# Kernel optimization log

Hardware: AMD Instinct MI355X
Metric: run time of the kernel (lower is better)

Reference implementation:

```python
import jax, jax.numpy as jnp
import numpy as np

B, N, ND, H = 8, 1024, 64, 128
NUM_OPS, NUM_PARAMS, SKETCH = 64, 256, 128


def setup_inputs() -> dict:
    key = jax.random.key(0)
    ks = iter(jax.random.split(key, 64))

    def rn(shape, s=0.05):
        return jax.random.normal(next(ks), shape, dtype=jnp.float32) * s

    inp = {
        'node_features': jax.random.normal(next(ks), (B, N, ND), dtype=jnp.float32),
        'adjacency': (jax.random.uniform(next(ks), (B, N, N)) < 0.05).astype(jnp.float32),
        'mask': jnp.ones((B, N), jnp.float32),
    }
    for name, din in (('g1', ND), ('g2', H), ('g3', H)):
        inp[name + '_W'] = rn((din, H))
        inp[name + '_b'] = jnp.zeros((H,), jnp.float32)
        inp[name + '_aW'] = rn((2 * H,))
        inp[name + '_ab'] = jnp.zeros((), jnp.float32)
    for l in (0, 1):
        inp[f'l{l}_Wih'] = rn((4 * H, H))
        inp[f'l{l}_Whh'] = rn((4 * H, H))
        inp[f'l{l}_bih'] = jnp.zeros((4 * H,), jnp.float32)
        inp[f'l{l}_bhh'] = jnp.zeros((4 * H,), jnp.float32)
    for name, dout in (('op', NUM_OPS), ('pa', NUM_PARAMS), ('sk', SKETCH), ('no', ND)):
        inp[name + '_W1'] = rn((H, H))
        inp[name + '_b1'] = jnp.zeros((H,), jnp.float32)
        inp[name + '_W2'] = rn((H, dout))
        inp[name + '_b2'] = jnp.zeros((dout,), jnp.float32)
    return inp


def _gnn(x, adj, W, b, aW, ab):
    # h = Linear(x); att[b,i,j] = sigmoid(aW . [h_j ; h_i] + ab)  (cat order from the torch code)
    h = x @ W + b                      # [B,N,H]
    D = W.shape[1]
    sj = h @ aW[:D]                    # contribution of the dim-1-expanded term (h_j)
    si = h @ aW[D:]                    # contribution of the dim-2-expanded term (h_i)
    att = jax.nn.sigmoid(si[:, :, None] + sj[:, None, :] + ab) * adj  # [B,N,N]
    return jnp.einsum('bij,bjd->bid', att, h)


def _lstm(x, Wih, Whh, bih, bhh):
    # single torch-style LSTM layer, gate order i,f,g,o; zero initial state
    Bx, Hh = x.shape[0], Whh.shape[1]

    def step(carry, xt):
        h, c = carry
        g = xt @ Wih.T + h @ Whh.T + (bih + bhh)       # [B,4H]
        i, f, gg, o = jnp.split(g, 4, axis=-1)
        c = jax.nn.sigmoid(f) * c + jax.nn.sigmoid(i) * jnp.tanh(gg)
        h = jax.nn.sigmoid(o) * jnp.tanh(c)
        return (h, c), h

    z = jnp.zeros((Bx, Hh), x.dtype)
    _, ys = jax.lax.scan(step, (z, z), jnp.swapaxes(x, 0, 1))
    return jnp.swapaxes(ys, 0, 1)


def _mlp(x, W1, b1, W2, b2):
    return jax.nn.relu(x @ W1 + b1) @ W2 + b2


def reference(node_features, adjacency, mask,
              g1_W, g1_b, g1_aW, g1_ab,
              g2_W, g2_b, g2_aW, g2_ab,
              g3_W, g3_b, g3_aW, g3_ab,
              l0_Wih, l0_Whh, l0_bih, l0_bhh,
              l1_Wih, l1_Whh, l1_bih, l1_bhh,
              op_W1, op_b1, op_W2, op_b2,
              pa_W1, pa_b1, pa_W2, pa_b2,
              sk_W1, sk_b1, sk_W2, sk_b2,
              no_W1, no_b1, no_W2, no_b2):
    h = jax.nn.relu(_gnn(node_features, adjacency, g1_W, g1_b, g1_aW, g1_ab))
    h = jax.nn.relu(_gnn(h, adjacency, g2_W, g2_b, g2_aW, g2_ab))
    h = _gnn(h, adjacency, g3_W, g3_b, g3_aW, g3_ab)
    lo = _lstm(h, l0_Wih, l0_Whh, l0_bih, l0_bhh)
    lo = _lstm(lo, l1_Wih, l1_Whh, l1_bih, l1_bhh)
    op_pred = _mlp(lo, op_W1, op_b1, op_W2, op_b2)
    param_pred = _mlp(lo, pa_W1, pa_b1, pa_W2, pa_b2)
    sketch_pred = _mlp(lo, sk_W1, sk_b1, sk_W2, sk_b2)
    node_pred = _mlp(h, no_W1, no_b1, no_W2, no_b2)
    return (op_pred, param_pred, sketch_pred, node_pred)
```

## Files before the change

### kernel.cpp

```cpp
#include <hip/hip_runtime.h>

typedef __attribute__((ext_vector_type(8))) short short8;
typedef __attribute__((ext_vector_type(4))) float f32x4;
typedef __attribute__((ext_vector_type(2))) float f32x2;
typedef __attribute__((ext_vector_type(4))) unsigned short us4;
typedef __attribute__((ext_vector_type(2))) unsigned int u32x2;

__device__ __forceinline__ unsigned short bf16_of(float f) {
    unsigned u = __builtin_bit_cast(unsigned, f);
    u += 0x7fffu + ((u >> 16) & 1u);
    return (unsigned short)(u >> 16);
}
__device__ __forceinline__ unsigned bf16pk(float a, float b) {
    return (unsigned)bf16_of(a) | ((unsigned)bf16_of(b) << 16);
}
__device__ __forceinline__ float fexp2(float x) { return __builtin_amdgcn_exp2f(x); }
__device__ __forceinline__ float frcp(float x) { return __builtin_amdgcn_rcpf(x); }
__device__ __forceinline__ float sigm(float x) { return frcp(1.f + fexp2(-1.44269504f * x)); }
__device__ __forceinline__ float tanh_f(float x) {
    float e = fexp2(2.88539008f * x);
    return 1.f - 2.f * frcp(e + 1.f);
}
__device__ __forceinline__ f32x4 mfma16(short8 a, short8 b, f32x4 c) {
    return __builtin_amdgcn_mfma_f32_16x16x32_bf16(a, b, c, 0, 0, 0);
}
__device__ __forceinline__ float dpp_shr8(float x) {
    return __builtin_bit_cast(float, __builtin_amdgcn_update_dpp(
        0, __builtin_bit_cast(int, x), 0x118, 0xF, 0xF, true));
}
__device__ __forceinline__ float dpp_shl8(float x) {
    return __builtin_bit_cast(float, __builtin_amdgcn_update_dpp(
        0, __builtin_bit_cast(int, x), 0x108, 0xF, 0xF, true));
}

__global__ __launch_bounds__(256) void gemm_f32(
    const float* __restrict__ A, const float* __restrict__ B,
    const float* __restrict__ bias, float* __restrict__ C,
    int M, int N, int K, int BT, int RELU, int PACK)
{
    __shared__ float As[64][33];
    __shared__ float Bs[32][68];
    const int tid = threadIdx.x;
    const int tx = tid & 15, ty = tid >> 4;
    const int m0 = blockIdx.y * 64, n0 = blockIdx.x * 64;
    float acc[4][4];
#pragma unroll
    for (int i = 0; i < 4; ++i)
#pragma unroll
        for (int j = 0; j < 4; ++j) acc[i][j] = 0.f;

    for (int k0 = 0; k0 < K; k0 += 32) {
        __syncthreads();
        {
            const int r = tid >> 2, kk = (tid & 3) * 8;
            const float* src = A + (size_t)(m0 + r) * K + k0 + kk;
            f32x4 v0 = *(const f32x4*)src;
            f32x4 v1 = *(const f32x4*)(src + 4);
#pragma unroll
            for (int e = 0; e < 4; ++e) { As[r][kk + e] = v0[e]; As[r][kk + 4 + e] = v1[e]; }
        }
        if (!BT) {
            const int kk = tid >> 3, nn = (tid & 7) * 8;
            const float* src = B + (size_t)(k0 + kk) * N + n0 + nn;
            f32x4 v0 = *(const f32x4*)src;
            f32x4 v1 = *(const f32x4*)(src + 4);
#pragma unroll
            for (int e = 0; e < 4; ++e) { Bs[kk][nn + e] = v0[e]; Bs[kk][nn + 4 + e] = v1[e]; }
        } else {
            const int n = tid >> 2, kk = (tid & 3) * 8;
            const float* src = B + (size_t)(n0 + n) * K + k0 + kk;
            f32x4 v0 = *(const f32x4*)src;
            f32x4 v1 = *(const f32x4*)(src + 4);
#pragma unroll
            for (int e = 0; e < 4; ++e) { Bs[kk + e][n] = v0[e]; Bs[kk + 4 + e][n] = v1[e]; }
        }
        __syncthreads();
#pragma unroll 8
        for (int k = 0; k < 32; ++k) {
            float a0 = As[ty * 4 + 0][k], a1 = As[ty * 4 + 1][k];
            float a2 = As[ty * 4 + 2][k], a3 = As[ty * 4 + 3][k];
            f32x4 bv = *(const f32x4*)&Bs[k][tx * 4];
#pragma unroll
            for (int j = 0; j < 4; ++j) {
                acc[0][j] += a0 * bv[j]; acc[1][j] += a1 * bv[j];
                acc[2][j] += a2 * bv[j]; acc[3][j] += a3 * bv[j];
            }
        }
    }
    f32x4 bv = {};
    if (bias != nullptr) bv = *(const f32x4*)&bias[n0 + tx * 4];
#pragma unroll
    for (int i = 0; i < 4; ++i) {
        f32x4 res = {};
#pragma unroll
        for (int j = 0; j < 4; ++j) {
            float v = acc[i][j] + bv[j];
            if (RELU) v = fmaxf(v, 0.f);
            res[j] = v;
        }
        const int m = m0 + ty * 4 + i;
        if (!PACK) {
            *(f32x4*)&C[(size_t)m * N + n0 + tx * 4] = res;
        } else {
            const int b = m >> 10, t = m & 1023;
            const int n = n0 + tx * 4;
            const int pr = n >> 7, h = n & 127;
            *(f32x4*)&C[(((size_t)t * 4 + pr) * 8 + b) * 128 + h] = res;
        }
    }
}

__global__ __launch_bounds__(256) void sisj_kernel(
    const float* __restrict__ h, const float* __restrict__ aW,
    float* __restrict__ si, float* __restrict__ sj)
{
    const int tid = threadIdx.x, lane = tid & 63, w = tid >> 6;
    const int row = blockIdx.x * 4 + w;
    f32x2 hv = *(const f32x2*)(h + (size_t)row * 128 + lane * 2);
    f32x2 w1 = *(const f32x2*)&aW[lane * 2];
    f32x2 w2 = *(const f32x2*)&aW[128 + lane * 2];
    float sjp = hv[0] * w1[0] + hv[1] * w1[1];
    float sip = hv[0] * w2[0] + hv[1] * w2[1];
#pragma unroll
    for (int o = 32; o > 0; o >>= 1) {
        sjp += __shfl_xor(sjp, o);
        sip += __shfl_xor(sip, o);
    }
    if (lane == 0) { si[row] = sip; sj[row] = sjp; }
}

__global__ __launch_bounds__(256) void transpose_bf16_k(
    const float* __restrict__ h, unsigned short* __restrict__ hT)
{
    __shared__ float t[64][65];
    const int b = blockIdx.z, jt = blockIdx.x, dt = blockIdx.y;
    const int tid = threadIdx.x;
    const int r = tid >> 4, c4 = (tid & 15) * 4;
#pragma unroll
    for (int rr = 0; rr < 4; ++rr) {
        const int j = rr * 16 + r;
        f32x4 v = *(const f32x4*)(h + ((size_t)b * 1024 + jt * 64 + j) * 128 + dt * 64 + c4);
#pragma unroll
        for (int e = 0; e < 4; ++e) t[j][c4 + e] = v[e];
    }
    __syncthreads();
#pragma unroll
    for (int rr = 0; rr < 4; ++rr) {
        const int d = rr * 16 + r;
        u32x2 o;
        o[0] = bf16pk(t[c4 + 0][d], t[c4 + 1][d]);
        o[1] = bf16pk(t[c4 + 2][d], t[c4 + 3][d]);
        *(u32x2*)(hT + ((size_t)b * 128 + dt * 64 + d) * 1024 + jt * 64 + c4) = o;
    }
}

__global__ __launch_bounds__(256) void gnn_agg(
    const float* __restrict__ adj, const unsigned short* __restrict__ hT,
    const float* __restrict__ si, const float* __restrict__ sj,
    const float* __restrict__ abp, float* __restrict__ out, int RELU)
{
    __shared__ __align__(16) unsigned short Alds[64 * 40];
    __shared__ __align__(16) unsigned short Blds[128 * 40];
    const int b = blockIdx.y, it = blockIdx.x;
    const int i0 = it * 64;
    const int tid = threadIdx.x, lane = tid & 63, w = tid >> 6;
    const int quad = lane >> 4, col = lane & 15;
    const float ab = abp[0];
    const float* adjb = adj + (size_t)b * 1024 * 1024;
    const unsigned short* hTb = hT + (size_t)b * 128 * 1024;
    const float* sjb = sj + b * 1024;

    f32x4 acc[8] = {};
    const int ar_ = tid >> 2, ash = (tid & 3) * 8;
    const int br_ = tid >> 1, bsh = (tid & 1) * 16;
    const float sii = si[b * 1024 + i0 + ar_] + ab;

    for (int j0 = 0; j0 < 1024; j0 += 32) {
        __syncthreads();
        {
            const float* ar = adjb + (size_t)(i0 + ar_) * 1024 + j0 + ash;
            f32x4 av0 = *(const f32x4*)ar;
            f32x4 av1 = *(const f32x4*)(ar + 4);
            float s[8];
#pragma unroll
            for (int e = 0; e < 4; ++e) {
                s[e]     = sigm(sii + sjb[j0 + ash + e])     * av0[e];
                s[4 + e] = sigm(sii + sjb[j0 + ash + 4 + e]) * av1[e];
            }
            u32x2 o0 = {bf16pk(s[0], s[1]), bf16pk(s[2], s[3])};
            u32x2 o1 = {bf16pk(s[4], s[5]), bf16pk(s[6], s[7])};
            unsigned short* al = Alds + ar_ * 40 + ash;
            *(u32x2*)&al[0] = o0;
            *(u32x2*)&al[4] = o1;
        }
        {
            const unsigned short* bsrc = hTb + (size_t)br_ * 1024 + j0 + bsh;
            unsigned short* bl = Blds + br_ * 40 + bsh;
            *(short8*)&bl[0] = *(const short8*)&bsrc[0];
            *(short8*)&bl[8] = *(const short8*)&bsrc[8];
        }
        __syncthreads();
        short8 af = *(const short8*)&Alds[(w * 16 + col) * 40 + quad * 8];
#pragma unroll
        for (int nt = 0; nt < 8; ++nt) {
            short8 bf = *(const short8*)&Blds[(nt * 16 + col) * 40 + quad * 8];
            acc[nt] = mfma16(af, bf, acc[nt]);
        }
    }
    const int ibase = i0 + w * 16 + quad * 4;
#pragma unroll
    for (int nt = 0; nt < 8; ++nt) {
        const int d = nt * 16 + col;
#pragma unroll
        for (int r = 0; r < 4; ++r) {
            float v = acc[nt][r];
            if (RELU) v = fmaxf(v, 0.f);
            out[((size_t)b * 1024 + ibase + r) * 128 + d] = v;
        }
    }
}

struct PrepArgs {
    const float* src[8];
    unsigned short* dst[8];
    int N[8];
};
__global__ __launch_bounds__(256) void prep_k(
    PrepArgs pa, const float* bih0, const float* bhh0,
    float* bsum, int* flags)
{
    const int m = blockIdx.x;
    const int tid = threadIdx.x;
    if (m < 8) {
        const float* src = pa.src[m];
        unsigned short* dst = pa.dst[m];
        const int N = pa.N[m];
        const int n0 = tid >> 4, kc = (tid & 15) * 8;
        for (int n = n0; n < N; n += 16) {
            unsigned o[4];
#pragma unroll
            for (int e = 0; e < 8; e += 2)
                o[e >> 1] = bf16pk(src[(size_t)(kc + e) * N + n],
                                   src[(size_t)(kc + e + 1) * N + n]);
            *(u32x2*)&dst[n * 128 + kc] = *(u32x2*)&o[0];
            *(u32x2*)&dst[n * 128 + kc + 4] = *(u32x2*)&o[2];
        }
    } else {
        bsum[tid] = bih0[tid] + bhh0[tid];
        bsum[tid + 256] = bih0[tid + 256] + bhh0[tid + 256];
        if (tid < 3) flags[tid] = 0;
    }
}


struct HeadArgs {
    const unsigned short* W1T[4];
    const float* b1[4];
    const unsigned short* W2T[4];
    const float* b2[4];
    float* outp[4];
};

__device__ __forceinline__ void lstm_epilogue(
    const f32x4 accs[4], f32x4 xv0, f32x4 xv1, float* cst, float* hv, bool lo)
{
    float t0[4], t1[4];
#pragma unroll
    for (int i = 0; i < 4; ++i) {
        float P0 = 0.5f * ((lo ? accs[0][i] : dpp_shr8(accs[1][i])) + xv0[i]);
        float P1r = (lo ? accs[2][i] : dpp_shr8(accs[3][i])) + xv1[i];
        float P1 = lo ? P1r : 0.5f * P1r;
        t0[i] = tanh_f(P0);
        t1[i] = tanh_f(P1);
    }
    float c2[4], og[4];
#pragma unroll
    for (int i = 0; i < 4; ++i) {
        float ig = 0.5f + 0.5f * t0[i];
        float fg = 0.5f + 0.5f * dpp_shl8(t0[i]);
        float gg = t1[i];
        og[i] = 0.5f + 0.5f * dpp_shl8(t1[i]);
        c2[i] = fg * cst[i] + ig * gg;
        cst[i] = c2[i];
    }
    float pc0 = lo ? c2[0] : dpp_shr8(c2[1]);
    float pc1 = lo ? c2[2] : dpp_shr8(c2[3]);
    float tc0 = tanh_f(pc0), tc1 = tanh_f(pc1);
    float th[4] = {tc0, dpp_shl8(tc0), tc1, dpp_shl8(tc1)};
#pragma unroll
    for (int i = 0; i < 4; ++i) hv[i] = og[i] * th[i];
}

template <int SINK>
__device__ __forceinline__ void lstm_step(
    unsigned short* Hc, unsigned short* Hn, const short8 afr[4][4],
    f32x4 xv0, f32x4 xv1, float* cst, unsigned short* __restrict__ sink,
    int t, int col, int quad, int h4, int b)
{
    short8 bfr[4];
#pragma unroll
    for (int c = 0; c < 4; ++c)
        bfr[c] = *(const short8*)&Hc[col * 136 + c * 32 + quad * 8];
    f32x4 accs[4] = {};
#pragma unroll
    for (int c = 0; c < 4; ++c)
#pragma unroll
        for (int g = 0; g < 4; ++g)
            accs[g] = mfma16(afr[g][c], bfr[c], accs[g]);

    const bool lo = (col < 8);
    float hv[4];
    lstm_epilogue(accs, xv0, xv1, cst, hv, lo);
    if (lo) {
        u32x2 hb = {bf16pk(hv[0], hv[1]), bf16pk(hv[2], hv[3])};
        *(u32x2*)&Hn[b * 136 + h4] = hb;
        if (SINK == 0)
            *(u32x2*)(sink + (size_t)t * 1024 + b * 128 + h4) = hb;
        else
            *(u32x2*)(sink + ((size_t)t * 8 + b) * 128 + h4) = hb;
    }
    __builtin_amdgcn_s_waitcnt(0xC07F);
    __builtin_amdgcn_s_barrier();
}

template <int A32, int LROWS>
__device__ void head_strip(
    const void* __restrict__ Asrc, int row0,
    const unsigned short* __restrict__ W1T, const float* __restrict__ b1,
    const unsigned short* __restrict__ W2T, const float* __restrict__ b2,
    float* __restrict__ outp, int dout, unsigned short* A2, int tid)
{
    const int lane = tid & 63, w = tid >> 6;
    const int quad = lane >> 4, col = lane & 15;
    const int mrow = w * 16 + col;
    f32x4 acc[8] = {};
#pragma unroll
    for (int kc = 0; kc < 4; ++kc) {
        short8 af;
        if (A32) {
            const float* s = (const float*)Asrc + (size_t)(row0 + mrow) * 128 + kc * 32 + quad * 8;
            f32x4 v0 = *(const f32x4*)s, v1 = *(const f32x4*)(s + 4);
            short8 v;
#pragma unroll
            for (int j = 0; j < 4; ++j) {
                v[j] = (short)bf16_of(v0[j]);
                v[4 + j] = (short)bf16_of(v1[j]);
            }
            af = v;
        } else {
            af = *(const short8*)((const unsigned short*)Asrc +
                                  (size_t)(row0 + mrow) * 128 + kc * 32 + quad * 8);
        }
#pragma unroll
        for (int nt = 0; nt < 8; ++nt) {
            short8 bf = *(const short8*)&W1T[(nt * 16 + col) * 128 + kc * 32 + quad * 8];
            acc[nt] = mfma16(af, bf, acc[nt]);
        }
    }
    float b1v[8];
#pragma unroll
    for (int nt = 0; nt < 8; ++nt) b1v[nt] = b1[nt * 16 + col];
    __syncthreads();
#pragma unroll
    for (int nt = 0; nt < 8; ++nt)
#pragma unroll
        for (int i = 0; i < 4; ++i) {
            const int mm = w * 16 + quad * 4 + i;
            A2[mm * 136 + nt * 16 + col] = bf16_of(fmaxf(acc[nt][i] + b1v[nt], 0.f));
        }
    __syncthreads();
    const int ntiles = dout >> 4;
    for (int np = 0; np < ntiles; np += 8) {
        const int nts = (ntiles - np < 8) ? ntiles - np : 8;
        f32x4 acc2[8] = {};
#pragma unroll
        for (int kc = 0; kc < 4; ++kc) {
            short8 a2f = *(const short8*)&A2[mrow * 136 + kc * 32 + quad * 8];
            for (int nt = 0; nt < nts; ++nt) {
                short8 bf = *(const short8*)&W2T[((np + nt) * 16 + col) * 128 + kc * 32 + quad * 8];
                acc2[nt] = mfma16(a2f, bf, acc2[nt]);
            }
        }
        for (int nt = 0; nt < nts; ++nt) {
            const int n = (np + nt) * 16 + col;
            const float bb = b2[n];
#pragma unroll
            for (int i = 0; i < 4; ++i) {
                const int r = row0 + w * 16 + quad * 4 + i;
                size_t off;
                if (LROWS) off = ((size_t)(r & 7) * 1024 + (r >> 3)) * dout + n;
                else       off = (size_t)r * dout + n;
                outp[off] = acc2[nt][i] + bb;
            }
        }
    }
}

__global__ __launch_bounds__(512) void lstm_pipe(
    const float* __restrict__ xw0, const float* __restrict__ Whh0,
    const float* __restrict__ Wih1, const float* __restrict__ Whh1,
    const float* __restrict__ bih1, const float* __restrict__ bhh1,
    unsigned short* __restrict__ hbuf, float* __restrict__ xw1,
    int* __restrict__ flags, unsigned short* __restrict__ out1b,
    const float* __restrict__ bufH3, HeadArgs ha)
{
    __shared__ __align__(16) unsigned short H[2][16 * 136];
    __shared__ __align__(16) unsigned short A2[128 * 136];
    const int tid = threadIdx.x;
    const int lane = tid & 63;
    const int w = tid >> 6;
    const int quad = lane >> 4;
    const int col = lane & 15;
    const int b = col & 7;
    const int prA = col >> 3;
    const int h4 = w * 16 + quad * 4;

    if (blockIdx.x >= 3) {
        const int wid = blockIdx.x - 3;
        for (int s = wid; s < 64; s += 8)
            head_strip<1, 0>(bufH3, s * 128, ha.W1T[3], ha.b1[3],
                             ha.W2T[3], ha.b2[3], ha.outp[3], 64, A2, tid);
        for (int s = wid; s < 64; s += 8) {
            if (tid == 0) {
                while (__hip_atomic_load(&flags[2], __ATOMIC_ACQUIRE,
                                         __HIP_MEMORY_SCOPE_AGENT) < s + 1)
                    __builtin_amdgcn_s_sleep(16);
            }
            __syncthreads();
            head_strip<0, 1>(out1b, s * 128, ha.W1T[0], ha.b1[0],
                             ha.W2T[0], ha.b2[0], ha.outp[0], 64, A2, tid);
            head_strip<0, 1>(out1b, s * 128, ha.W1T[1], ha.b1[1],
                             ha.W2T[1], ha.b2[1], ha.outp[1], 256, A2, tid);
            head_strip<0, 1>(out1b, s * 128, ha.W1T[2], ha.b1[2],
                             ha.W2T[2], ha.b2[2], ha.outp[2], 128, A2, tid);
        }
        return;
    }

    if (blockIdx.x == 1) {
        short8 afrI[4][4];
        f32x4 biasv[4];
#pragma unroll
        for (int g = 0; g < 4; ++g) {
            const int row = g * 128 + w * 16 + col;
#pragma unroll
            for (int c = 0; c < 4; ++c) {
                const float* src = Wih1 + row * 128 + c * 32 + quad * 8;
                short8 v;
#pragma unroll
                for (int j = 0; j < 8; ++j) v[j] = (short)bf16_of(src[j]);
                afrI[g][c] = v;
            }
            const int rb = g * 128 + w * 16 + quad * 4;
            f32x4 b1 = *(const f32x4*)&bih1[rb];
            f32x4 b2 = *(const f32x4*)&bhh1[rb];
#pragma unroll
            for (int e = 0; e < 4; ++e) biasv[g][e] = b1[e] + b2[e];
        }
        for (int k = 0; k < 64; ++k) {
            if (tid == 0) {
                while (__hip_atomic_load(&flags[0], __ATOMIC_ACQUIRE,
                                         __HIP_MEMORY_SCOPE_AGENT) < k + 1)
                    __builtin_amdgcn_s_sleep(2);
                if (k >= 4) {
                    while (__hip_atomic_load(&flags[2], __ATOMIC_RELAXED,
                                             __HIP_MEMORY_SCOPE_AGENT) < k - 3)
                        __builtin_amdgcn_s_sleep(2);
                }
            }
            __builtin_amdgcn_s_waitcnt(0xC07F);
            __builtin_amdgcn_s_barrier();
            const unsigned short* hb = hbuf + (size_t)k * 16 * 1024;
            float* dst = xw1 + (size_t)(k & 3) * 65536;
#pragma unroll 2
            for (int nt = 0; nt < 8; ++nt) {
                const int tl = nt * 2 + (col >> 3);
                const unsigned short* src = hb + tl * 1024 + b * 128 + quad * 8;
                short8 bfr[4];
#pragma unroll
                for (int c = 0; c < 4; ++c) bfr[c] = *(const short8*)&src[c * 32];
                f32x4 acc[4] = {};
#pragma unroll
                for (int c = 0; c < 4; ++c)
#pragma unroll
                    for (int g = 0; g < 4; ++g)
                        acc[g] = mfma16(afrI[g][c], bfr[c], acc[g]);
#pragma unroll
                for (int g = 0; g < 4; ++g) {
                    f32x4 res;
#pragma unroll
                    for (int e = 0; e < 4; ++e) res[e] = acc[g][e] + biasv[g][e];
                    *(f32x4*)&dst[((tl * 4 + g) * 8 + b) * 128 + w * 16 + quad * 4] = res;
                }
            }
            __builtin_amdgcn_s_waitcnt(0x0F70);
            __builtin_amdgcn_s_barrier();
            if (tid == 0)
                __hip_atomic_store(&flags[1], k + 1, __ATOMIC_RELEASE,
                                   __HIP_MEMORY_SCOPE_AGENT);
        }
        return;
    }

    for (int i = tid; i < 2 * 16 * 136; i += 512) (&H[0][0])[i] = 0;
    float cst[4] = {0.f, 0.f, 0.f, 0.f};
    const int lane_off = (prA * 8 + b) * 128 + h4;

    if (blockIdx.x == 0) {
        short8 afr[4][4];
#pragma unroll
        for (int g = 0; g < 4; ++g) {
            const int row = g * 128 + w * 16 + col;
#pragma unroll
            for (int c = 0; c < 4; ++c) {
                const float* src = Whh0 + row * 128 + c * 32 + quad * 8;
                short8 v;
#pragma unroll
                for (int j = 0; j < 8; ++j) v[j] = (short)bf16_of(src[j]);
                afr[g][c] = v;
            }
        }
        const float* xp = xw0 + lane_off;
        f32x4 p0a = *(const f32x4*)(xp);
        f32x4 p1a = *(const f32x4*)(xp + 2048);
        f32x4 p0b = *(const f32x4*)(xp + 4096);
        f32x4 p1b = *(const f32x4*)(xp + 6144);
        xp += 8192;
        __syncthreads();

        for (int t = 0; t < 1024; t += 2) {
            const float* xr = (t == 1022) ? xp - 8192 : xp;
            {
                f32x4 xv0 = p0a, xv1 = p1a;
                p0a = *(const f32x4*)(xr);
                p1a = *(const f32x4*)(xr + 2048);
                lstm_step<0>(&H[0][0], &H[1][0], afr, xv0, xv1, cst, hbuf, t, col, quad, h4, b);
            }
            {
                f32x4 xv0 = p0b, xv1 = p1b;
                p0b = *(const f32x4*)(xr + 4096);
                p1b = *(const f32x4*)(xr + 6144);
                lstm_step<0>(&H[1][0], &H[0][0], afr, xv0, xv1, cst, hbuf, t + 1, col, quad, h4, b);
            }
            xp += 8192;
            if ((t & 14) == 14) {
                __syncthreads();
                if (tid == 0)
                    __hip_atomic_store(&flags[0], (t >> 4) + 1, __ATOMIC_RELEASE,
                                       __HIP_MEMORY_SCOPE_AGENT);
            }
        }
    } else {
        short8 afr[4][4];
#pragma unroll
        for (int g = 0; g < 4; ++g) {
            const int row = g * 128 + w * 16 + col;
#pragma unroll
            for (int c = 0; c < 4; ++c) {
                const float* src = Whh1 + row * 128 + c * 32 + quad * 8;
                short8 v;
#pragma unroll
                for (int j = 0; j < 8; ++j) v[j] = (short)bf16_of(src[j]);
                afr[g][c] = v;
            }
        }
        __syncthreads();
        auto xaddr = [&](int t) -> const float* {
            return xw1 + (((t >> 4) & 3) * 65536 + (t & 15) * 4096) + lane_off;
        };
        while (__hip_atomic_load(&flags[1], __ATOMIC_ACQUIRE,
                                 __HIP_MEMORY_SCOPE_AGENT) < 2)
            __builtin_amdgcn_s_sleep(2);
        f32x4 p0a = *(const f32x4*)xaddr(0);
        f32x4 p1a = *(const f32x4*)(xaddr(0) + 2048);
        f32x4 p0b = *(const f32x4*)xaddr(1);
        f32x4 p1b = *(const f32x4*)(xaddr(1) + 2048);

        for (int c = 0; c < 64; ++c) {
            if (c > 0) {
                const int target = (c + 2 < 64) ? c + 2 : 64;
                if (tid == 0) {
                    while (__hip_atomic_load(&flags[1], __ATOMIC_ACQUIRE,
                                             __HIP_MEMORY_SCOPE_AGENT) < target)
                        __builtin_amdgcn_s_sleep(2);
                }
                __builtin_amdgcn_s_waitcnt(0xC07F);
                __builtin_amdgcn_s_barrier();
            }
            for (int s = 0; s < 16; s += 2) {
                const int t = c * 16 + s;
                const int t2 = (t + 2 < 1024) ? t + 2 : 1023;
                const int t3 = (t + 3 < 1024) ? t + 3 : 1023;
                {
                    f32x4 xv0 = p0a, xv1 = p1a;
                    p0a = *(const f32x4*)xaddr(t2);
                    p1a = *(const f32x4*)(xaddr(t2) + 2048);
                    lstm_step<1>(&H[0][0], &H[1][0], afr, xv0, xv1, cst, out1b, t, col, quad, h4, b);
                }
                {
                    f32x4 xv0 = p0b, xv1 = p1b;
                    p0b = *(const f32x4*)xaddr(t3);
                    p1b = *(const f32x4*)(xaddr(t3) + 2048);
                    lstm_step<1>(&H[1][0], &H[0][0], afr, xv0, xv1, cst, out1b, t + 1, col, quad, h4, b);
                }
            }
            __syncthreads();
            if (tid == 0)
                __hip_atomic_store(&flags[2], c + 1, __ATOMIC_RELEASE,
                                   __HIP_MEMORY_SCOPE_AGENT);
        }
    }
}

extern "C" void kernel_launch(void* const* d_in, const int* in_sizes, int n_in,
                              void* d_out, int out_size, void* d_ws, size_t ws_size,
                              hipStream_t stream)
{
    (void)in_sizes; (void)n_in; (void)out_size; (void)ws_size;
    const float* nf    = (const float*)d_in[0];
    const float* adj   = (const float*)d_in[1];
    const float* g1W   = (const float*)d_in[3];
    const float* g1b   = (const float*)d_in[4];
    const float* g1aW  = (const float*)d_in[5];
    const float* g1ab  = (const float*)d_in[6];
    const float* g2W   = (const float*)d_in[7];
    const float* g2b   = (const float*)d_in[8];
    const float* g2aW  = (const float*)d_in[9];
    const float* g2ab  = (const float*)d_in[10];
    const float* g3W   = (const float*)d_in[11];
    const float* g3b   = (const float*)d_in[12];
    const float* g3aW  = (const float*)d_in[13];
    const float* g3ab  = (const float*)d_in[14];
    const float* l0Wih = (const float*)d_in[15];
    const float* l0Whh = (const float*)d_in[16];
    const float* l0bih = (const float*)d_in[17];
    const float* l0bhh = (const float*)d_in[18];
    const float* l1Wih = (const float*)d_in[19];
    const float* l1Whh = (const float*)d_in[20];
    const float* l1bih = (const float*)d_in[21];
    const float* l1bhh = (const float*)d_in[22];
    const float* opW1 = (const float*)d_in[23];
    const float* opb1 = (const float*)d_in[24];
    const float* opW2 = (const float*)d_in[25];
    const float* opb2 = (const float*)d_in[26];
    const float* paW1 = (const float*)d_in[27];
    const float* pab1 = (const float*)d_in[28];
    const float* paW2 = (const float*)d_in[29];
    const float* pab2 = (const float*)d_in[30];
    const float* skW1 = (const float*)d_in[31];
    const float* skb1 = (const float*)d_in[32];
    const float* skW2 = (const float*)d_in[33];
    const float* skb2 = (const float*)d_in[34];
    const float* noW1 = (const float*)d_in[35];
    const float* nob1 = (const float*)d_in[36];
    const float* noW2 = (const float*)d_in[37];
    const float* nob2 = (const float*)d_in[38];

    float* out = (float*)d_out;
    float* ws = (float*)d_ws;
    float* bufH  = ws;
    float* bufX  = ws + 1048576;
    float* bufH3 = ws + 2097152;
    unsigned short* bufT = (unsigned short*)(ws + 3145728);
    float* siB  = ws + 3670016;
    float* sjB  = ws + 3678208;
    float* bsum = ws + 3686400;
    float* xw0  = ws + 3687424;
    float* xw1  = ws + 7881728;
    int*  flags = (int*)(ws + 8143872);
    unsigned short* WT = (unsigned short*)(ws + 8143876);
    unsigned short* out1b = (unsigned short*)(ws + 8209412);
    unsigned short* hbuf = (unsigned short*)bufX;

    unsigned short* opW1T = WT;
    unsigned short* paW1T = WT + 16384;
    unsigned short* skW1T = WT + 32768;
    unsigned short* noW1T = WT + 49152;
    unsigned short* opW2T = WT + 65536;
    unsigned short* paW2T = WT + 73728;
    unsigned short* skW2T = WT + 106496;
    unsigned short* noW2T = WT + 122880;

    auto gemm = [&](const float* A, const float* B, const float* bias, float* C,
                    int M, int N, int K, int BT, int RELU, int PACK = 0) {
        dim3 g(N / 64, M / 64);
        gemm_f32<<<g, dim3(256), 0, stream>>>(A, B, bias, C, M, N, K, BT, RELU, PACK);
    };

    gemm(nf, g1W, g1b, bufH, 8192, 128, 64, 0, 0);
    sisj_kernel<<<2048, 256, 0, stream>>>(bufH, g1aW, siB, sjB);
    transpose_bf16_k<<<dim3(16, 2, 8), 256, 0, stream>>>(bufH, bufT);
    gnn_agg<<<dim3(16, 8), 256, 0, stream>>>(adj, bufT, siB, sjB, g1ab, bufX, 1);
    gemm(bufX, g2W, g2b, bufH, 8192, 128, 128, 0, 0);
    sisj_kernel<<<2048, 256, 0, stream>>>(bufH, g2aW, siB, sjB);
    transpose_bf16_k<<<dim3(16, 2, 8), 256, 0, stream>>>(bufH, bufT);
    gnn_agg<<<dim3(16, 8), 256, 0, stream>>>(adj, bufT, siB, sjB, g2ab, bufX, 1);
    gemm(bufX, g3W, g3b, bufH, 8192, 128, 128, 0, 0);
    sisj_kernel<<<2048, 256, 0, stream>>>(bufH, g3aW, siB, sjB);
    transpose_bf16_k<<<dim3(16, 2, 8), 256, 0, stream>>>(bufH, bufT);
    gnn_agg<<<dim3(16, 8), 256, 0, stream>>>(adj, bufT, siB, sjB, g3ab, bufH3, 0);

    PrepArgs pargs;
    pargs.src[0] = opW1; pargs.dst[0] = opW1T; pargs.N[0] = 128;
    pargs.src[1] = paW1; pargs.dst[1] = paW1T; pargs.N[1] = 128;
    pargs.src[2] = skW1; pargs.dst[2] = skW1T; pargs.N[2] = 128;
    pargs.src[3] = noW1; pargs.dst[3] = noW1T; pargs.N[3] = 128;
    pargs.src[4] = opW2; pargs.dst[4] = opW2T; pargs.N[4] = 64;
    pargs.src[5] = paW2; pargs.dst[5] = paW2T; pargs.N[5] = 256;
    pargs.src[6] = skW2; pargs.dst[6] = skW2T; pargs.N[6] = 128;
    pargs.src[7] = noW2; pargs.dst[7] = noW2T; pargs.N[7] = 64;
    prep_k<<<9, 256, 0, stream>>>(pargs, l0bih, l0bhh, bsum, flags);

    gemm(bufH3, l0Wih, bsum, xw0, 8192, 512, 128, 1, 0, 1);

    HeadArgs ha;
    ha.W1T[0] = opW1T; ha.b1[0] = opb1; ha.W2T[0] = opW2T; ha.b2[0] = opb2;
    ha.outp[0] = out + 0;
    ha.W1T[1] = paW1T; ha.b1[1] = pab1; ha.W2T[1] = paW2T; ha.b2[1] = pab2;
    ha.outp[1] = out + 524288;
    ha.W1T[2] = skW1T; ha.b1[2] = skb1; ha.W2T[2] = skW2T; ha.b2[2] = skb2;
    ha.outp[2] = out + 2621440;
    ha.W1T[3] = noW1T; ha.b1[3] = nob1; ha.W2T[3] = noW2T; ha.b2[3] = nob2;
    ha.outp[3] = out + 3670016;
    lstm_pipe<<<11, 512, 0, stream>>>(xw0, l0Whh, l1Wih, l1Whh, l1bih, l1bhh,
                                      hbuf, xw1, flags, out1b, bufH3, ha);
}
```

Measured before the change: 1.426 ms.

## Fuse GNN linear with score and bf16 transpose, pipeline aggregation, simplify LSTM gates

Merges each GNN layer's linear GEMM, attention-score reductions and bf16 transpose into one kernel that writes per-column-block partial si/sj. This drops the intermediate fp32 h buffer and two launches per layer. The aggregation kernel now uses 32-row tiles, caches sj in LDS and double-buffers adjacency and hT loads in registers, giving twice as many blocks. The LSTM epilogue computes sigmoid and tanh directly, with weight and bias pre-scaling for one gate, in place of the tanh-based half-angle trick, which changes numerics slightly.

```diff
diff --git a/kernel.cpp b/kernel.cpp
--- a/kernel.cpp
+++ b/kernel.cpp
@@ -2,8 +2,6 @@
 
 typedef __attribute__((ext_vector_type(8))) short short8;
 typedef __attribute__((ext_vector_type(4))) float f32x4;
-typedef __attribute__((ext_vector_type(2))) float f32x2;
-typedef __attribute__((ext_vector_type(4))) unsigned short us4;
 typedef __attribute__((ext_vector_type(2))) unsigned int u32x2;
 
 __device__ __forceinline__ unsigned short bf16_of(float f) {
@@ -17,10 +15,6 @@
 __device__ __forceinline__ float fexp2(float x) { return __builtin_amdgcn_exp2f(x); }
 __device__ __forceinline__ float frcp(float x) { return __builtin_amdgcn_rcpf(x); }
 __device__ __forceinline__ float sigm(float x) { return frcp(1.f + fexp2(-1.44269504f * x)); }
-__device__ __forceinline__ float tanh_f(float x) {
-    float e = fexp2(2.88539008f * x);
-    return 1.f - 2.f * frcp(e + 1.f);
-}
 __device__ __forceinline__ f32x4 mfma16(short8 a, short8 b, f32x4 c) {
     return __builtin_amdgcn_mfma_f32_16x16x32_bf16(a, b, c, 0, 0, 0);
 }
@@ -105,112 +99,199 @@
             const int b = m >> 10, t = m & 1023;
             const int n = n0 + tx * 4;
             const int pr = n >> 7, h = n & 127;
+            if (pr == 3) {
+#pragma unroll
+                for (int j = 0; j < 4; ++j) res[j] *= 0.5f;
+            }
             *(f32x4*)&C[(((size_t)t * 4 + pr) * 8 + b) * 128 + h] = res;
         }
     }
 }
 
-__global__ __launch_bounds__(256) void sisj_kernel(
-    const float* __restrict__ h, const float* __restrict__ aW,
-    float* __restrict__ si, float* __restrict__ sj)
+__global__ __launch_bounds__(256) void gemm_gnn(
+    const float* __restrict__ A, const float* __restrict__ B,
+    const float* __restrict__ bias, const float* __restrict__ aW,
+    unsigned short* __restrict__ hT, float* __restrict__ siP,
+    float* __restrict__ sjP, int K)
 {
-    const int tid = threadIdx.x, lane = tid & 63, w = tid >> 6;
-    const int row = blockIdx.x * 4 + w;
-    f32x2 hv = *(const f32x2*)(h + (size_t)row * 128 + lane * 2);
-    f32x2 w1 = *(const f32x2*)&aW[lane * 2];
-    f32x2 w2 = *(const f32x2*)&aW[128 + lane * 2];
-    float sjp = hv[0] * w1[0] + hv[1] * w1[1];
-    float sip = hv[0] * w2[0] + hv[1] * w2[1];
-#pragma unroll
-    for (int o = 32; o > 0; o >>= 1) {
-        sjp += __shfl_xor(sjp, o);
-        sip += __shfl_xor(sip, o);
-    }
-    if (lane == 0) { si[row] = sip; sj[row] = sjp; }
-}
-
-__global__ __launch_bounds__(256) void transpose_bf16_k(
-    const float* __restrict__ h, unsigned short* __restrict__ hT)
-{
-    __shared__ float t[64][65];
-    const int b = blockIdx.z, jt = blockIdx.x, dt = blockIdx.y;
+    __shared__ float As[64][33];
+    __shared__ float Bs[32][68];
+    __shared__ unsigned short T[64][70];
     const int tid = threadIdx.x;
+    const int tx = tid & 15, ty = tid >> 4;
+    const int m0 = blockIdx.y * 64, n0 = blockIdx.x * 64;
+    float acc[4][4];
+#pragma unroll
+    for (int i = 0; i < 4; ++i)
+#pragma unroll
+        for (int j = 0; j < 4; ++j) acc[i][j] = 0.f;
+
+    for (int k0 = 0; k0 < K; k0 += 32) {
+        __syncthreads();
+        {
+            const int r = tid >> 2, kk = (tid & 3) * 8;
+            const float* src = A + (size_t)(m0 + r) * K + k0 + kk;
+            f32x4 v0 = *(const f32x4*)src;
+            f32x4 v1 = *(const f32x4*)(src + 4);
+#pragma unroll
+            for (int e = 0; e < 4; ++e) { As[r][kk + e] = v0[e]; As[r][kk + 4 + e] = v1[e]; }
+        }
+        {
+            const int kk = tid >> 3, nn = (tid & 7) * 8;
+            const float* src = B + (size_t)(k0 + kk) * 128 + n0 + nn;
+            f32x4 v0 = *(const f32x4*)src;
+            f32x4 v1 = *(const f32x4*)(src + 4);
+#pragma unroll
+            for (int e = 0; e < 4; ++e) { Bs[kk][nn + e] = v0[e]; Bs[kk][nn + 4 + e] = v1[e]; }
+        }
+        __syncthreads();
+#pragma unroll 8
+        for (int k = 0; k < 32; ++k) {
+            float a0 = As[ty * 4 + 0][k], a1 = As[ty * 4 + 1][k];
+            float a2 = As[ty * 4 + 2][k], a3 = As[ty * 4 + 3][k];
+            f32x4 bv = *(const f32x4*)&Bs[k][tx * 4];
+#pragma unroll
+            for (int j = 0; j < 4; ++j) {
+                acc[0][j] += a0 * bv[j]; acc[1][j] += a1 * bv[j];
+                acc[2][j] += a2 * bv[j]; acc[3][j] += a3 * bv[j];
+            }
+        }
+    }
+    f32x4 bv = *(const f32x4*)&bias[n0 + tx * 4];
+#pragma unroll
+    for (int i = 0; i < 4; ++i)
+#pragma unroll
+        for (int j = 0; j < 4; ++j) acc[i][j] += bv[j];
+
+    f32x4 wj = *(const f32x4*)&aW[n0 + tx * 4];
+    f32x4 wi = *(const f32x4*)&aW[128 + n0 + tx * 4];
+#pragma unroll
+    for (int i = 0; i < 4; ++i) {
+        float pj = acc[i][0] * wj[0] + acc[i][1] * wj[1] + acc[i][2] * wj[2] + acc[i][3] * wj[3];
+        float pi = acc[i][0] * wi[0] + acc[i][1] * wi[1] + acc[i][2] * wi[2] + acc[i][3] * wi[3];
+#pragma unroll
+        for (int o = 8; o > 0; o >>= 1) {
+            pj += __shfl_xor(pj, o);
+            pi += __shfl_xor(pi, o);
+        }
+        if (tx == 0) {
+            const int m = m0 + ty * 4 + i;
+            sjP[blockIdx.x * 8192 + m] = pj;
+            siP[blockIdx.x * 8192 + m] = pi;
+        }
+    }
+
+#pragma unroll
+    for (int i = 0; i < 4; ++i) {
+        unsigned* tp = (unsigned*)&T[ty * 4 + i][tx * 4];
+        tp[0] = bf16pk(acc[i][0], acc[i][1]);
+        tp[1] = bf16pk(acc[i][2], acc[i][3]);
+    }
+    __syncthreads();
+    const int b = m0 >> 10, node0 = m0 & 1023;
     const int r = tid >> 4, c4 = (tid & 15) * 4;
-#pragma unroll
-    for (int rr = 0; rr < 4; ++rr) {
-        const int j = rr * 16 + r;
-        f32x4 v = *(const f32x4*)(h + ((size_t)b * 1024 + jt * 64 + j) * 128 + dt * 64 + c4);
-#pragma unroll
-        for (int e = 0; e < 4; ++e) t[j][c4 + e] = v[e];
-    }
-    __syncthreads();
 #pragma unroll
     for (int rr = 0; rr < 4; ++rr) {
         const int d = rr * 16 + r;
         u32x2 o;
-        o[0] = bf16pk(t[c4 + 0][d], t[c4 + 1][d]);
-        o[1] = bf16pk(t[c4 + 2][d], t[c4 + 3][d]);
-        *(u32x2*)(hT + ((size_t)b * 128 + dt * 64 + d) * 1024 + jt * 64 + c4) = o;
+        o[0] = (unsigned)T[c4 + 0][d] | ((unsigned)T[c4 + 1][d] << 16);
+        o[1] = (unsigned)T[c4 + 2][d] | ((unsigned)T[c4 + 3][d] << 16);
+        *(u32x2*)(hT + ((size_t)b * 128 + n0 + d) * 1024 + node0 + c4) = o;
     }
 }
 
 __global__ __launch_bounds__(256) void gnn_agg(
     const float* __restrict__ adj, const unsigned short* __restrict__ hT,
-    const float* __restrict__ si, const float* __restrict__ sj,
+    const float* __restrict__ siP, const float* __restrict__ sjP,
     const float* __restrict__ abp, float* __restrict__ out, int RELU)
 {
-    __shared__ __align__(16) unsigned short Alds[64 * 40];
+    __shared__ __align__(16) unsigned short Alds[32 * 40];
     __shared__ __align__(16) unsigned short Blds[128 * 40];
+    __shared__ float sjL[1024];
     const int b = blockIdx.y, it = blockIdx.x;
-    const int i0 = it * 64;
+    const int i0 = it * 32;
     const int tid = threadIdx.x, lane = tid & 63, w = tid >> 6;
     const int quad = lane >> 4, col = lane & 15;
+    const int rh = w & 1, nh = w >> 1;
     const float ab = abp[0];
     const float* adjb = adj + (size_t)b * 1024 * 1024;
     const unsigned short* hTb = hT + (size_t)b * 128 * 1024;
-    const float* sjb = sj + b * 1024;
-
-    f32x4 acc[8] = {};
-    const int ar_ = tid >> 2, ash = (tid & 3) * 8;
+
+    for (int j = tid; j < 1024; j += 256)
+        sjL[j] = sjP[b * 1024 + j] + sjP[8192 + b * 1024 + j];
+
+    const int ar_ = tid >> 3, ash = (tid & 7) * 4;
     const int br_ = tid >> 1, bsh = (tid & 1) * 16;
-    const float sii = si[b * 1024 + i0 + ar_] + ab;
-
-    for (int j0 = 0; j0 < 1024; j0 += 32) {
+    const float sii = siP[b * 1024 + i0 + ar_] + siP[8192 + b * 1024 + i0 + ar_] + ab;
+
+    const float* aptr = adjb + (size_t)(i0 + ar_) * 1024 + ash;
+    const unsigned short* bptr = hTb + (size_t)br_ * 1024 + bsh;
+
+    f32x4 paA = *(const f32x4*)(aptr);
+    short8 pbA0 = *(const short8*)(bptr);
+    short8 pbA1 = *(const short8*)(bptr + 8);
+    f32x4 paB = *(const f32x4*)(aptr + 32);
+    short8 pbB0 = *(const short8*)(bptr + 32);
+    short8 pbB1 = *(const short8*)(bptr + 40);
+
+    f32x4 acc[4] = {};
+
+    for (int j0 = 0; j0 < 1024; j0 += 64) {
         __syncthreads();
         {
-            const float* ar = adjb + (size_t)(i0 + ar_) * 1024 + j0 + ash;
-            f32x4 av0 = *(const f32x4*)ar;
-            f32x4 av1 = *(const f32x4*)(ar + 4);
-            float s[8];
-#pragma unroll
-            for (int e = 0; e < 4; ++e) {
-                s[e]     = sigm(sii + sjb[j0 + ash + e])     * av0[e];
-                s[4 + e] = sigm(sii + sjb[j0 + ash + 4 + e]) * av1[e];
-            }
-            u32x2 o0 = {bf16pk(s[0], s[1]), bf16pk(s[2], s[3])};
-            u32x2 o1 = {bf16pk(s[4], s[5]), bf16pk(s[6], s[7])};
-            unsigned short* al = Alds + ar_ * 40 + ash;
-            *(u32x2*)&al[0] = o0;
-            *(u32x2*)&al[4] = o1;
-        }
+            float s0 = sigm(sii + sjL[j0 + ash + 0]) * paA[0];
+            float s1 = sigm(sii + sjL[j0 + ash + 1]) * paA[1];
+            float s2 = sigm(sii + sjL[j0 + ash + 2]) * paA[2];
+            float s3 = sigm(sii + sjL[j0 + ash + 3]) * paA[3];
+            u32x2 o = {bf16pk(s0, s1), bf16pk(s2, s3)};
+            *(u32x2*)&Alds[ar_ * 40 + ash] = o;
+            *(short8*)&Blds[br_ * 40 + bsh] = pbA0;
+            *(short8*)&Blds[br_ * 40 + bsh + 8] = pbA1;
+        }
+        if (j0 + 64 < 1024) {
+            paA = *(const f32x4*)(aptr + j0 + 64);
+            pbA0 = *(const short8*)(bptr + j0 + 64);
+            pbA1 = *(const short8*)(bptr + j0 + 72);
+        }
+        __syncthreads();
         {
-            const unsigned short* bsrc = hTb + (size_t)br_ * 1024 + j0 + bsh;
-            unsigned short* bl = Blds + br_ * 40 + bsh;
-            *(short8*)&bl[0] = *(const short8*)&bsrc[0];
-            *(short8*)&bl[8] = *(const short8*)&bsrc[8];
-        }
-        __syncthreads();
-        short8 af = *(const short8*)&Alds[(w * 16 + col) * 40 + quad * 8];
-#pragma unroll
-        for (int nt = 0; nt < 8; ++nt) {
-            short8 bf = *(const short8*)&Blds[(nt * 16 + col) * 40 + quad * 8];
-            acc[nt] = mfma16(af, bf, acc[nt]);
-        }
-    }
-    const int ibase = i0 + w * 16 + quad * 4;
-#pragma unroll
-    for (int nt = 0; nt < 8; ++nt) {
-        const int d = nt * 16 + col;
+            short8 af = *(const short8*)&Alds[(rh * 16 + col) * 40 + quad * 8];
+#pragma unroll
+            for (int nt = 0; nt < 4; ++nt) {
+                short8 bf = *(const short8*)&Blds[((nh * 4 + nt) * 16 + col) * 40 + quad * 8];
+                acc[nt] = mfma16(af, bf, acc[nt]);
+            }
+        }
+        __syncthreads();
+        {
+            float s0 = sigm(sii + sjL[j0 + 32 + ash + 0]) * paB[0];
+            float s1 = sigm(sii + sjL[j0 + 32 + ash + 1]) * paB[1];
+            float s2 = sigm(sii + sjL[j0 + 32 + ash + 2]) * paB[2];
+            float s3 = sigm(sii + sjL[j0 + 32 + ash + 3]) * paB[3];
+            u32x2 o = {bf16pk(s0, s1), bf16pk(s2, s3)};
+            *(u32x2*)&Alds[ar_ * 40 + ash] = o;
+            *(short8*)&Blds[br_ * 40 + bsh] = pbB0;
+            *(short8*)&Blds[br_ * 40 + bsh + 8] = pbB1;
+        }
+        if (j0 + 96 < 1024) {
+            paB = *(const f32x4*)(aptr + j0 + 96);
+            pbB0 = *(const short8*)(bptr + j0 + 96);
+            pbB1 = *(const short8*)(bptr + j0 + 104);
+        }
+        __syncthreads();
+        {
+            short8 af = *(const short8*)&Alds[(rh * 16 + col) * 40 + quad * 8];
+#pragma unroll
+            for (int nt = 0; nt < 4; ++nt) {
+                short8 bf = *(const short8*)&Blds[((nh * 4 + nt) * 16 + col) * 40 + quad * 8];
+                acc[nt] = mfma16(af, bf, acc[nt]);
+            }
+        }
+    }
+    const int ibase = i0 + rh * 16 + quad * 4;
+#pragma unroll
+    for (int nt = 0; nt < 4; ++nt) {
+        const int d = (nh * 4 + nt) * 16 + col;
 #pragma unroll
         for (int r = 0; r < 4; ++r) {
             float v = acc[nt][r];
@@ -262,30 +343,37 @@
 };
 
 __device__ __forceinline__ void lstm_epilogue(
-    const f32x4 accs[4], f32x4 xv0, f32x4 xv1, float* cst, float* hv, bool lo)
+    const f32x4 accs[4], f32x4 xv0, f32x4 xv1, float* cst, float* hv,
+    bool lo, float selLo)
 {
     float t0[4], t1[4];
 #pragma unroll
     for (int i = 0; i < 4; ++i) {
-        float P0 = 0.5f * ((lo ? accs[0][i] : dpp_shr8(accs[1][i])) + xv0[i]);
-        float P1r = (lo ? accs[2][i] : dpp_shr8(accs[3][i])) + xv1[i];
-        float P1 = lo ? P1r : 0.5f * P1r;
-        t0[i] = tanh_f(P0);
-        t1[i] = tanh_f(P1);
+        float P0 = (lo ? accs[0][i] : dpp_shr8(accs[1][i])) + xv0[i];
+        float P1 = (lo ? accs[2][i] : dpp_shr8(accs[3][i])) + xv1[i];
+        P1 = fmaxf(P1, -30.f);
+        t0[i] = frcp(1.f + fexp2(-1.44269504f * P0));
+        float u = fexp2(-2.88539008f * P1);
+        t1[i] = (1.f - selLo * u) * frcp(1.f + u);
     }
     float c2[4], og[4];
 #pragma unroll
     for (int i = 0; i < 4; ++i) {
-        float ig = 0.5f + 0.5f * t0[i];
-        float fg = 0.5f + 0.5f * dpp_shl8(t0[i]);
+        float ig = t0[i];
+        float fg = dpp_shl8(t0[i]);
         float gg = t1[i];
-        og[i] = 0.5f + 0.5f * dpp_shl8(t1[i]);
+        og[i] = dpp_shl8(t1[i]);
         c2[i] = fg * cst[i] + ig * gg;
         cst[i] = c2[i];
     }
     float pc0 = lo ? c2[0] : dpp_shr8(c2[1]);
     float pc1 = lo ? c2[2] : dpp_shr8(c2[3]);
-    float tc0 = tanh_f(pc0), tc1 = tanh_f(pc1);
+    pc0 = fmaxf(pc0, -30.f);
+    pc1 = fmaxf(pc1, -30.f);
+    float u0 = fexp2(-2.88539008f * pc0);
+    float tc0 = (1.f - u0) * frcp(1.f + u0);
+    float u1 = fexp2(-2.88539008f * pc1);
+    float tc1 = (1.f - u1) * frcp(1.f + u1);
     float th[4] = {tc0, dpp_shl8(tc0), tc1, dpp_shl8(tc1)};
 #pragma unroll
     for (int i = 0; i < 4; ++i) hv[i] = og[i] * th[i];
@@ -309,8 +397,9 @@
             accs[g] = mfma16(afr[g][c], bfr[c], accs[g]);
 
     const bool lo = (col < 8);
+    const float selLo = lo ? 1.f : 0.f;
     float hv[4];
-    lstm_epilogue(accs, xv0, xv1, cst, hv, lo);
+    lstm_epilogue(accs, xv0, xv1, cst, hv, lo, selLo);
     if (lo) {
         u32x2 hb = {bf16pk(hv[0], hv[1]), bf16pk(hv[2], hv[3])};
         *(u32x2*)&Hn[b * 136 + h4] = hb;
@@ -442,20 +531,21 @@
         f32x4 biasv[4];
 #pragma unroll
         for (int g = 0; g < 4; ++g) {
+            const float gsc = (g == 3) ? 0.5f : 1.f;
             const int row = g * 128 + w * 16 + col;
 #pragma unroll
             for (int c = 0; c < 4; ++c) {
                 const float* src = Wih1 + row * 128 + c * 32 + quad * 8;
                 short8 v;
 #pragma unroll
-                for (int j = 0; j < 8; ++j) v[j] = (short)bf16_of(src[j]);
+                for (int j = 0; j < 8; ++j) v[j] = (short)bf16_of(src[j] * gsc);
                 afrI[g][c] = v;
             }
             const int rb = g * 128 + w * 16 + quad * 4;
             f32x4 b1 = *(const f32x4*)&bih1[rb];
             f32x4 b2 = *(const f32x4*)&bhh1[rb];
 #pragma unroll
-            for (int e = 0; e < 4; ++e) biasv[g][e] = b1[e] + b2[e];
+            for (int e = 0; e < 4; ++e) biasv[g][e] = (b1[e] + b2[e]) * gsc;
         }
         for (int k = 0; k < 64; ++k) {
             if (tid == 0) {
@@ -510,13 +600,14 @@
         short8 afr[4][4];
 #pragma unroll
         for (int g = 0; g < 4; ++g) {
+            const float gsc = (g == 3) ? 0.5f : 1.f;
             const int row = g * 128 + w * 16 + col;
 #pragma unroll
             for (int c = 0; c < 4; ++c) {
                 const float* src = Whh0 + row * 128 + c * 32 + quad * 8;
                 short8 v;
 #pragma unroll
-                for (int j = 0; j < 8; ++j) v[j] = (short)bf16_of(src[j]);
+                for (int j = 0; j < 8; ++j) v[j] = (short)bf16_of(src[j] * gsc);
                 afr[g][c] = v;
             }
         }
@@ -554,13 +645,14 @@
         short8 afr[4][4];
 #pragma unroll
         for (int g = 0; g < 4; ++g) {
+            const float gsc = (g == 3) ? 0.5f : 1.f;
             const int row = g * 128 + w * 16 + col;
 #pragma unroll
             for (int c = 0; c < 4; ++c) {
                 const float* src = Whh1 + row * 128 + c * 32 + quad * 8;
                 short8 v;
 #pragma unroll
-                for (int j = 0; j < 8; ++j) v[j] = (short)bf16_of(src[j]);
+                for (int j = 0; j < 8; ++j) v[j] = (short)bf16_of(src[j] * gsc);
                 afr[g][c] = v;
             }
         }
@@ -658,12 +750,11 @@
 
     float* out = (float*)d_out;
     float* ws = (float*)d_ws;
-    float* bufH  = ws;
+    float* siP   = ws;
+    float* sjP   = ws + 16384;
     float* bufX  = ws + 1048576;
     float* bufH3 = ws + 2097152;
     unsigned short* bufT = (unsigned short*)(ws + 3145728);
-    float* siB  = ws + 3670016;
-    float* sjB  = ws + 3678208;
     float* bsum = ws + 3686400;
     float* xw0  = ws + 3687424;
     float* xw1  = ws + 7881728;
@@ -681,24 +772,12 @@
     unsigned short* skW2T = WT + 106496;
     unsigned short* noW2T = WT + 122880;
 
-    auto gemm = [&](const float* A, const float* B, const float* bias, float* C,
-                    int M, int N, int K, int BT, int RELU, int PACK = 0) {
-        dim3 g(N / 64, M / 64);
-        gemm_f32<<<g, dim3(256), 0, stream>>>(A, B, bias, C, M, N, K, BT, RELU, PACK);
-    };
-
-    gemm(nf, g1W, g1b, bufH, 8192, 128, 64, 0, 0);
-    sisj_kernel<<<2048, 256, 0, stream>>>(bufH, g1aW, siB, sjB);
-    transpose_bf16_k<<<dim3(16, 2, 8), 256, 0, stream>>>(bufH, bufT);
-    gnn_agg<<<dim3(16, 8), 256, 0, stream>>>(adj, bufT, siB, sjB, g1ab, bufX, 1);
-    gemm(bufX, g2W, g2b, bufH, 8192, 128, 128, 0, 0);
-    sisj_kernel<<<2048, 256, 0, stream>>>(bufH, g2aW, siB, sjB);
-    transpose_bf16_k<<<dim3(16, 2, 8), 256, 0, stream>>>(bufH, bufT);
-    gnn_agg<<<dim3(16, 8), 256, 0, stream>>>(adj, bufT, siB, sjB, g2ab, bufX, 1);
-    gemm(bufX, g3W, g3b, bufH, 8192, 128, 128, 0, 0);
-    sisj_kernel<<<2048, 256, 0, stream>>>(bufH, g3aW, siB, sjB);
-    transpose_bf16_k<<<dim3(16, 2, 8), 256, 0, stream>>>(bufH, bufT);
-    gnn_agg<<<dim3(16, 8), 256, 0, stream>>>(adj, bufT, siB, sjB, g3ab, bufH3, 0);
+    gemm_gnn<<<dim3(2, 128), 256, 0, stream>>>(nf, g1W, g1b, g1aW, bufT, siP, sjP, 64);
+    gnn_agg<<<dim3(32, 8), 256, 0, stream>>>(adj, bufT, siP, sjP, g1ab, bufX, 1);
+    gemm_gnn<<<dim3(2, 128), 256, 0, stream>>>(bufX, g2W, g2b, g2aW, bufT, siP, sjP, 128);
+    gnn_agg<<<dim3(32, 8), 256, 0, stream>>>(adj, bufT, siP, sjP, g2ab, bufX, 1);
+    gemm_gnn<<<dim3(2, 128), 256, 0, stream>>>(bufX, g3W, g3b, g3aW, bufT, siP, sjP, 128);
+    gnn_agg<<<dim3(32, 8), 256, 0, stream>>>(adj, bufT, siP, sjP, g3ab, bufH3, 0);
 
     PrepArgs pargs;
     pargs.src[0] = opW1; pargs.dst[0] = opW1T; pargs.N[0] = 128;
@@ -711,7 +790,11 @@
     pargs.src[7] = noW2; pargs.dst[7] = noW2T; pargs.N[7] = 64;
     prep_k<<<9, 256, 0, stream>>>(pargs, l0bih, l0bhh, bsum, flags);
 
-    gemm(bufH3, l0Wih, bsum, xw0, 8192, 512, 128, 1, 0, 1);
+    {
+        dim3 g(512 / 64, 8192 / 64);
+        gemm_f32<<<g, dim3(256), 0, stream>>>(bufH3, l0Wih, bsum, xw0,
+                                              8192, 512, 128, 1, 0, 1);
+    }
 
     HeadArgs ha;
     ha.W1T[0] = opW1T; ha.b1[0] = opb1; ha.W2T[0] = opW2T; ha.b2[0] = opb2;
```

Result: faster. 1.346 ms (-5.6%).
